# Kernel tuning notes

Measured on AMD Instinct MI355X. Metric: run time of the kernel, lower is better.

## Reference

```python
import jax, jax.numpy as jnp
import numpy as np

B, N, F_IN, F_OUT, NUM_TYPES = 16, 16384, 128, 128, 16

def setup_inputs() -> dict:
    key = jax.random.key(0)
    k1, k2, k3, k4 = jax.random.split(key, 4)
    x = jax.random.normal(k1, (B, N, F_IN), dtype=jnp.float32)
    type_vec = jax.random.randint(k2, (N,), 0, NUM_TYPES, dtype=jnp.int64)
    # torch.nn.Linear weight layout: [out_features, in_features]
    bound = 1.0 / np.sqrt(F_IN)
    W = jax.random.uniform(k3, (NUM_TYPES, F_OUT, F_IN), dtype=jnp.float32,
                           minval=-bound, maxval=bound)
    b = jax.random.uniform(k4, (NUM_TYPES, F_OUT), dtype=jnp.float32,
                           minval=-bound, maxval=bound)
    return {"x": x, "type_vec": type_vec, "W": W, "b": b}

def reference(x, type_vec, W, b):
    # Per-node weight gather then batched matvec: exact math of
    # out[:, n] = x[:, n] @ W[type_vec[n]].T + b[type_vec[n]]
    Wn = W[type_vec]          # [N, F_out, F_in]
    bn = b[type_vec]          # [N, F_out]
    out = jnp.einsum('bni,noi->bno', x, Wn) + bn  # [B, N, F_out]
    return out
```

## Files before the change

### kernel.cpp

```cpp
#include <hip/hip_runtime.h>
#include <hip/hip_bf16.h>


#define NN 16384
#define FF 128
#define NT 16
#define NPB 4
#define NBLK (NN / NPB + NT)
#define PB 64
#define WS_PORD 64
#define WS_BH (WS_PORD + NBLK * NPB)

typedef __bf16 bf16x8 __attribute__((ext_vector_type(8)));
typedef float  f32x4  __attribute__((ext_vector_type(4)));


__global__ __launch_bounds__(256) void hl_hist(const int* __restrict__ tv,
                                               int* __restrict__ ws) {
    __shared__ int wh[4][NT];
    const int tid = threadIdx.x, lane = tid & 63, wv = tid >> 6;
    const int t = tv[blockIdx.x * 256 + tid];
#pragma unroll
    for (int ty = 0; ty < NT; ++ty) {
        const unsigned long long m = __ballot(t == ty);
        if (lane == 0) wh[wv][ty] = __popcll(m);
    }
    __syncthreads();
    if (tid < NT)
        ws[WS_BH + tid * PB + blockIdx.x] = wh[0][tid] + wh[1][tid] + wh[2][tid] + wh[3][tid];
}

__global__ __launch_bounds__(256) void hl_scatter(const int* __restrict__ tv,
                                                  int* __restrict__ ws) {
    __shared__ int bh[NT * PB];
    __shared__ int scnt[NT], mybase[NT], sblk[NT + 1];
    __shared__ int wh[4][NT], wbase[4][NT];
    const int tid = threadIdx.x, lane = tid & 63, wv = tid >> 6;

    for (int i = tid; i < NT * PB; i += 256) bh[i] = ws[WS_BH + i];

    const int n = blockIdx.x * 256 + tid;
    const int t = tv[n];
    int myrank = 0;
#pragma unroll
    for (int ty = 0; ty < NT; ++ty) {
        const unsigned long long m = __ballot(t == ty);
        if (lane == 0) wh[wv][ty] = __popcll(m);
        if (t == ty) myrank = __popcll(m & ((1ull << lane) - 1ull));
    }
    __syncthreads();
    if (tid < NT) {
        int acc = 0, myb = 0;
        for (int b = 0; b < PB; ++b) {
            if (b == (int)blockIdx.x) myb = acc;
            acc += bh[tid * PB + b];
        }
        scnt[tid] = acc;
        mybase[tid] = myb;
    }
    __syncthreads();
    if (tid == 0) {
        int bacc = 0;
        for (int ty = 0; ty < NT; ++ty) {
            sblk[ty] = bacc;
            bacc += (scnt[ty] + NPB - 1) / NPB;
        }
        sblk[NT] = bacc;
        if (blockIdx.x == 0) ws[48] = bacc;
    }
    __syncthreads();
    if (tid < NT) {
        int base = sblk[tid] * NPB + mybase[tid];
        for (int w = 0; w < 4; ++w) { wbase[w][tid] = base; base += wh[w][tid]; }
    }
    __syncthreads();
    ws[WS_PORD + wbase[wv][t] + myrank] = (t << 20) | n;

    if (blockIdx.x == 0 && tid < NT) {
        const int lo = sblk[tid] * NPB + scnt[tid];
        const int hi = sblk[tid + 1] * NPB;
        for (int s = lo; s < hi; ++s) ws[WS_PORD + s] = (tid << 20) | 0x10000;
    }
}

__global__ __launch_bounds__(512, 4) void hl_main(
    const float* __restrict__ x,
    const float* __restrict__ W,
    const float* __restrict__ bias,
    const int*   __restrict__ ws,
    float*       __restrict__ out)
{
    const int lane = threadIdx.x & 63;
    const int wvid = threadIdx.x >> 6;
    const int p    = wvid >> 1;
    const int h    = wvid & 1;
    const int bid  = blockIdx.x;

    const int e = ws[WS_PORD + bid * NPB + p];
    if (bid >= ws[48]) return;

    const int  t = e >> 20;
    const bool v = !(e & 0x10000);
    const int  n = e & 0x3FFF;

    const int lrow = lane & 15;
    const int lgrp = lane >> 4;

    const float* xbase = x + (size_t)lrow * ((size_t)NN * FF) + lgrp * 8;
    f32x4 xv[8];
#pragma unroll
    for (int kk = 0; kk < 4; ++kk) {
        const float* xp = xbase + (size_t)n * FF + kk * 32;
        xv[2 * kk]     = *(const f32x4*)xp;
        xv[2 * kk + 1] = *(const f32x4*)(xp + 4);
    }

    float bv[4];
#pragma unroll
    for (int ot = 0; ot < 4; ++ot) bv[ot] = bias[t * FF + (h * 4 + ot) * 16 + lrow];

    __shared__ __align__(16) unsigned char Wl[FF * 256];
    const float* Wt = W + t * (FF * FF);
#pragma unroll
    for (int ii = 0; ii < 4; ++ii) {
        const int idx = ii * 512 + threadIdx.x;
        const float* ptr = Wt + idx * 8;
        f32x4 a = *(const f32x4*)ptr;
        f32x4 b = *(const f32x4*)(ptr + 4);
        bf16x8 vv;
#pragma unroll
        for (int j = 0; j < 4; ++j) { vv[j] = (__bf16)a[j]; vv[4 + j] = (__bf16)b[j]; }
        const int o  = idx >> 4;
        const int cb = (idx & 15) << 4;
        *(bf16x8*)(Wl + o * 256 + (cb ^ ((o & 7) << 4))) = vv;
    }
    __syncthreads();

    bf16x8 ahi[4], alo[4];
#pragma unroll
    for (int kk = 0; kk < 4; ++kk) {
#pragma unroll
        for (int j = 0; j < 4; ++j) {
            const float f0 = xv[2 * kk][j], f1 = xv[2 * kk + 1][j];
            const __bf16 h0 = (__bf16)f0, h1 = (__bf16)f1;
            ahi[kk][j]     = h0;  alo[kk][j]     = (__bf16)(f0 - (float)h0);
            ahi[kk][4 + j] = h1;  alo[kk][4 + j] = (__bf16)(f1 - (float)h1);
        }
    }

    f32x4 acc[4];
#pragma unroll
    for (int ot = 0; ot < 4; ++ot) acc[ot] = (f32x4){0.f, 0.f, 0.f, 0.f};
#pragma unroll
    for (int kk = 0; kk < 4; ++kk) {
#pragma unroll
        for (int ot = 0; ot < 4; ++ot) {
            const int o  = (h * 4 + ot) * 16 + lrow;
            const int cb = (kk * 64 + lgrp * 16) ^ ((o & 7) << 4);
            const bf16x8 wf = *(const bf16x8*)(Wl + o * 256 + cb);
            acc[ot] = __builtin_amdgcn_mfma_f32_16x16x32_bf16(ahi[kk], wf, acc[ot], 0, 0, 0);
            acc[ot] = __builtin_amdgcn_mfma_f32_16x16x32_bf16(alo[kk], wf, acc[ot], 0, 0, 0);
        }
    }

    if (v) {
#pragma unroll
        for (int ot = 0; ot < 4; ++ot) {
            const int o = (h * 4 + ot) * 16 + lrow;
#pragma unroll
            for (int r = 0; r < 4; ++r) {
                out[(size_t)(lgrp * 4 + r) * ((size_t)NN * FF) + (size_t)n * FF + o]
                    = acc[ot][r] + bv[ot];
            }
        }
    }
}

extern "C" void kernel_launch(void* const* d_in, const int* in_sizes, int n_in,
                              void* d_out, int out_size, void* d_ws, size_t ws_size,
                              hipStream_t stream) {
    const float* x    = (const float*)d_in[0];
    const int*   tv   = (const int*)d_in[1];
    const float* W    = (const float*)d_in[2];
    const float* bias = (const float*)d_in[3];
    float*       out  = (float*)d_out;
    int*         wsI  = (int*)d_ws;

    hl_hist<<<PB, 256, 0, stream>>>(tv, wsI);
    hl_scatter<<<PB, 256, 0, stream>>>(tv, wsI);
    hl_main<<<NBLK, 512, 0, stream>>>(x, W, bias, wsI, out);
}
```

Baseline: 75.75 us.

## Process 32 nodes per block with software-pipelined x loads per wave

Each block now handles 32 same-type nodes instead of 4, with each wave processing four nodes sequentially over all 128 outputs. The per-type weight tile is converted to bf16 into LDS once and reused across more nodes, which cuts redundant W reads and conversions and reduces the block count. The next node's x rows are prefetched into double-buffered registers while the current node's MFMAs run, with scheduling barriers to keep the overlap. The cost is more padding per type segment (up to 31 wasted node slots per type), higher register pressure, and fewer blocks for load balancing.

```diff
diff --git a/kernel.cpp b/kernel.cpp
--- a/kernel.cpp
+++ b/kernel.cpp
@@ -5,7 +5,7 @@
 #define NN 16384
 #define FF 128
 #define NT 16
-#define NPB 4
+#define NPB 32
 #define NBLK (NN / NPB + NT)
 #define PB 64
 #define WS_PORD 64
@@ -83,6 +83,54 @@
     }
 }
 
+#define LOAD_X(XV, N)                                                        \
+    _Pragma("unroll")                                                        \
+    for (int kk = 0; kk < 4; ++kk) {                                         \
+        const float* xp = xbase + (size_t)(N) * FF + kk * 32;                \
+        XV[2 * kk]     = *(const f32x4*)xp;                                  \
+        XV[2 * kk + 1] = *(const f32x4*)(xp + 4);                            \
+    }
+
+#define CVT_SPLIT(XV)                                                        \
+    _Pragma("unroll")                                                        \
+    for (int kk = 0; kk < 4; ++kk) {                                         \
+        _Pragma("unroll")                                                    \
+        for (int j = 0; j < 4; ++j) {                                        \
+            const float f0 = XV[2 * kk][j], f1 = XV[2 * kk + 1][j];          \
+            const __bf16 h0 = (__bf16)f0, h1 = (__bf16)f1;                   \
+            ahi[kk][j]     = h0;  alo[kk][j]     = (__bf16)(f0 - (float)h0); \
+            ahi[kk][4 + j] = h1;  alo[kk][4 + j] = (__bf16)(f1 - (float)h1); \
+        }                                                                    \
+    }
+
+#define COMPUTE_HALF(N, V, H)                                                \
+    {                                                                        \
+        f32x4 acc[4];                                                        \
+        _Pragma("unroll")                                                    \
+        for (int ot = 0; ot < 4; ++ot) acc[ot] = (f32x4){0.f, 0.f, 0.f, 0.f};\
+        _Pragma("unroll")                                                    \
+        for (int kk = 0; kk < 4; ++kk) {                                     \
+            _Pragma("unroll")                                                \
+            for (int ot = 0; ot < 4; ++ot) {                                 \
+                const int o  = ((H) * 4 + ot) * 16 + lrow;                   \
+                const int cb = (kk * 64 + lgrp * 16) ^ ((o & 7) << 4);       \
+                const bf16x8 wf = *(const bf16x8*)(Wl + o * 256 + cb);       \
+                acc[ot] = __builtin_amdgcn_mfma_f32_16x16x32_bf16(ahi[kk], wf, acc[ot], 0, 0, 0); \
+                acc[ot] = __builtin_amdgcn_mfma_f32_16x16x32_bf16(alo[kk], wf, acc[ot], 0, 0, 0); \
+            }                                                                \
+        }                                                                    \
+        if (V) {                                                             \
+            _Pragma("unroll")                                                \
+            for (int ot = 0; ot < 4; ++ot) {                                 \
+                const int o = ((H) * 4 + ot) * 16 + lrow;                    \
+                _Pragma("unroll")                                            \
+                for (int r = 0; r < 4; ++r)                                  \
+                    out[(size_t)(lgrp * 4 + r) * ((size_t)NN * FF)           \
+                        + (size_t)(N) * FF + o] = acc[ot][r] + bv[(H) * 4 + ot]; \
+            }                                                                \
+        }                                                                    \
+    }
+
 __global__ __launch_bounds__(512, 4) void hl_main(
     const float* __restrict__ x,
     const float* __restrict__ W,
@@ -91,42 +139,40 @@
     float*       __restrict__ out)
 {
     const int lane = threadIdx.x & 63;
-    const int wvid = threadIdx.x >> 6;
-    const int p    = wvid >> 1;
-    const int h    = wvid & 1;
+    const int wv   = threadIdx.x >> 6;
     const int bid  = blockIdx.x;
 
-    const int e = ws[WS_PORD + bid * NPB + p];
+    const int4 e4 = *(const int4*)&ws[WS_PORD + bid * NPB + wv * 4];
     if (bid >= ws[48]) return;
 
-    const int  t = e >> 20;
-    const bool v = !(e & 0x10000);
-    const int  n = e & 0x3FFF;
+    const int  t  = e4.x >> 20;
+    const int  n0 = e4.x & 0x3FFF, n1 = e4.y & 0x3FFF;
+    const int  n2 = e4.z & 0x3FFF, n3 = e4.w & 0x3FFF;
+    const bool v0 = !(e4.x & 0x10000), v1 = !(e4.y & 0x10000);
+    const bool v2 = !(e4.z & 0x10000), v3 = !(e4.w & 0x10000);
 
     const int lrow = lane & 15;
     const int lgrp = lane >> 4;
 
     const float* xbase = x + (size_t)lrow * ((size_t)NN * FF) + lgrp * 8;
-    f32x4 xv[8];
-#pragma unroll
-    for (int kk = 0; kk < 4; ++kk) {
-        const float* xp = xbase + (size_t)n * FF + kk * 32;
-        xv[2 * kk]     = *(const f32x4*)xp;
-        xv[2 * kk + 1] = *(const f32x4*)(xp + 4);
-    }
-
-    float bv[4];
-#pragma unroll
-    for (int ot = 0; ot < 4; ++ot) bv[ot] = bias[t * FF + (h * 4 + ot) * 16 + lrow];
+
+    f32x4  xvA[8], xvB[8];
+    bf16x8 ahi[4], alo[4];
+
+    LOAD_X(xvA, n0);
+
+    float bv[8];
+#pragma unroll
+    for (int ot = 0; ot < 8; ++ot) bv[ot] = bias[t * FF + ot * 16 + lrow];
 
     __shared__ __align__(16) unsigned char Wl[FF * 256];
     const float* Wt = W + t * (FF * FF);
 #pragma unroll
     for (int ii = 0; ii < 4; ++ii) {
         const int idx = ii * 512 + threadIdx.x;
-        const float* ptr = Wt + idx * 8;
-        f32x4 a = *(const f32x4*)ptr;
-        f32x4 b = *(const f32x4*)(ptr + 4);
+        const float* p = Wt + idx * 8;
+        f32x4 a = *(const f32x4*)p;
+        f32x4 b = *(const f32x4*)(p + 4);
         bf16x8 vv;
 #pragma unroll
         for (int j = 0; j < 4; ++j) { vv[j] = (__bf16)a[j]; vv[4 + j] = (__bf16)b[j]; }
@@ -136,44 +182,27 @@
     }
     __syncthreads();
 
-    bf16x8 ahi[4], alo[4];
-#pragma unroll
-    for (int kk = 0; kk < 4; ++kk) {
-#pragma unroll
-        for (int j = 0; j < 4; ++j) {
-            const float f0 = xv[2 * kk][j], f1 = xv[2 * kk + 1][j];
-            const __bf16 h0 = (__bf16)f0, h1 = (__bf16)f1;
-            ahi[kk][j]     = h0;  alo[kk][j]     = (__bf16)(f0 - (float)h0);
-            ahi[kk][4 + j] = h1;  alo[kk][4 + j] = (__bf16)(f1 - (float)h1);
-        }
-    }
-
-    f32x4 acc[4];
-#pragma unroll
-    for (int ot = 0; ot < 4; ++ot) acc[ot] = (f32x4){0.f, 0.f, 0.f, 0.f};
-#pragma unroll
-    for (int kk = 0; kk < 4; ++kk) {
-#pragma unroll
-        for (int ot = 0; ot < 4; ++ot) {
-            const int o  = (h * 4 + ot) * 16 + lrow;
-            const int cb = (kk * 64 + lgrp * 16) ^ ((o & 7) << 4);
-            const bf16x8 wf = *(const bf16x8*)(Wl + o * 256 + cb);
-            acc[ot] = __builtin_amdgcn_mfma_f32_16x16x32_bf16(ahi[kk], wf, acc[ot], 0, 0, 0);
-            acc[ot] = __builtin_amdgcn_mfma_f32_16x16x32_bf16(alo[kk], wf, acc[ot], 0, 0, 0);
-        }
-    }
-
-    if (v) {
-#pragma unroll
-        for (int ot = 0; ot < 4; ++ot) {
-            const int o = (h * 4 + ot) * 16 + lrow;
-#pragma unroll
-            for (int r = 0; r < 4; ++r) {
-                out[(size_t)(lgrp * 4 + r) * ((size_t)NN * FF) + (size_t)n * FF + o]
-                    = acc[ot][r] + bv[ot];
-            }
-        }
-    }
+    CVT_SPLIT(xvA);
+    LOAD_X(xvB, n1);
+    __builtin_amdgcn_sched_barrier(0);
+    COMPUTE_HALF(n0, v0, 0);
+    COMPUTE_HALF(n0, v0, 1);
+
+    CVT_SPLIT(xvB);
+    LOAD_X(xvA, n2);
+    __builtin_amdgcn_sched_barrier(0);
+    COMPUTE_HALF(n1, v1, 0);
+    COMPUTE_HALF(n1, v1, 1);
+
+    CVT_SPLIT(xvA);
+    LOAD_X(xvB, n3);
+    __builtin_amdgcn_sched_barrier(0);
+    COMPUTE_HALF(n2, v2, 0);
+    COMPUTE_HALF(n2, v2, 1);
+
+    CVT_SPLIT(xvB);
+    COMPUTE_HALF(n3, v3, 0);
+    COMPUTE_HALF(n3, v3, 1);
 }
 
 extern "C" void kernel_launch(void* const* d_in, const int* in_sizes, int n_in,
```

Result: faster. 73.44 us (-3.0%).
